# Kernel tuning notes

Measured on AMD Instinct MI355X. Metric: run time of the kernel, lower is better.

Reference implementation:

```python
import jax, jax.numpy as jnp
import numpy as np

B, S, D, H, FF = 4, 1024, 1024, 16, 4096
DH = D // H
EPS = 1e-5  # torch LayerNorm default


def _layernorm(x, g, b):
    m = jnp.mean(x, axis=-1, keepdims=True)
    v = jnp.mean((x - m) ** 2, axis=-1, keepdims=True)
    return (x - m) * jax.lax.rsqrt(v + EPS) * g + b


def setup_inputs() -> dict:
    key = jax.random.key(0)
    ks = jax.random.split(key, 8)
    init = lambda k, shape: jax.random.normal(k, shape, jnp.float32) * 0.02
    return {
        "x": jax.random.normal(ks[0], (B, S, D), jnp.float32),
        "Wq": init(ks[1], (D, D)), "bq": jnp.zeros((D,), jnp.float32),
        "Wk": init(ks[2], (D, D)), "bk": jnp.zeros((D,), jnp.float32),
        "Wv": init(ks[3], (D, D)), "bv": jnp.zeros((D,), jnp.float32),
        "Wo": init(ks[4], (D, D)), "bo": jnp.zeros((D,), jnp.float32),
        "ln1_g": jnp.ones((D,), jnp.float32), "ln1_b": jnp.zeros((D,), jnp.float32),
        "W1": init(ks[5], (D, FF)), "b1": jnp.zeros((FF,), jnp.float32),
        "W2": init(ks[6], (FF, D)), "b2": jnp.zeros((D,), jnp.float32),
        "ln2_g": jnp.ones((D,), jnp.float32), "ln2_b": jnp.zeros((D,), jnp.float32),
    }


def reference(x, Wq, bq, Wk, bk, Wv, bv, Wo, bo,
              ln1_g, ln1_b, W1, b1, W2, b2, ln2_g, ln2_b):
    Bx, Sx, _ = x.shape

    def heads(w, b):  # [B,S,D] -> [B,H,S,DH]
        return (x @ w + b).reshape(Bx, Sx, H, DH).transpose(0, 2, 1, 3)

    q, k, v = heads(Wq, bq), heads(Wk, bk), heads(Wv, bv)
    scores = jnp.einsum('bhqd,bhkd->bhqk', q, k) / jnp.sqrt(jnp.float32(DH))
    causal = jnp.tril(jnp.ones((Sx, Sx), bool))
    scores = jnp.where(causal[None, None], scores, jnp.float32(-1e9))
    attn = jax.nn.softmax(scores, axis=-1)           # [B,H,S,S]
    ctx = jnp.einsum('bhqk,bhkd->bqhd', attn, v).reshape(Bx, Sx, D)
    attn_out = ctx @ Wo + bo
    h = _layernorm(x + attn_out, ln1_g, ln1_b)
    ff = jax.nn.relu(h @ W1 + b1) @ W2 + b2
    y = _layernorm(h + ff, ln2_g, ln2_b)
    return (y, attn)
```

## Files before the change

### kernel.cpp

```cpp
#include <hip/hip_runtime.h>
#include <cstdint>


#define T_B 4
#define T_S 1024
#define T_D 1024
#define T_H 16
#define T_DH 64
#define T_FF 4096
#define T_TOK (T_B * T_S)

typedef __attribute__((ext_vector_type(8))) short bf16x8;
typedef __attribute__((ext_vector_type(4))) float f32x4;

__device__ __forceinline__ short f2bf(float f) {
  uint32_t u = __float_as_uint(f);
  u += 0x7FFFu + ((u >> 16) & 1u);
  return (short)(u >> 16);
}

__device__ __forceinline__ float bf2f(short s) {
  return __uint_as_float(((uint32_t)(unsigned short)s) << 16);
}

__device__ __forceinline__ void async_copy16(void* lds, const void* g) {
  __builtin_amdgcn_global_load_lds(
      (__attribute__((address_space(1))) uint32_t*)(uintptr_t)g,
      (__attribute__((address_space(3))) uint32_t*)(uint32_t)(uintptr_t)lds,
      16, 0, 0);
}

__device__ __forceinline__ void stage_ring(char* base, const char* gA0,
                                           const char* gA1, const char* gB0,
                                           const char* gB1, int koffB, int wid) {
  async_copy16(base + (wid << 10), gA0 + koffB);
  async_copy16(base + 4096 + (wid << 10), gA1 + koffB);
  async_copy16(base + 8192 + (wid << 10), gB0 + koffB);
  async_copy16(base + 12288 + (wid << 10), gB1 + koffB);
}

__device__ __forceinline__ void compute32(const short* As, const short* Bs,
                                          int wm, int wn, int quad, int r16,
                                          f32x4 acc[4][4]) {
  bf16x8 av[4], bv[4];
#pragma unroll
  for (int i = 0; i < 4; ++i) {
    av[i] = *(const bf16x8*)(As + ((wm + i * 16 + r16) << 5) + (quad << 3));
    bv[i] = *(const bf16x8*)(Bs + ((wn + i * 16 + r16) << 5) + (quad << 3));
  }
#pragma unroll
  for (int mi = 0; mi < 4; ++mi)
#pragma unroll
    for (int ni = 0; ni < 4; ++ni)
      acc[mi][ni] = __builtin_amdgcn_mfma_f32_16x16x32_bf16(av[mi], bv[ni],
                                                            acc[mi][ni], 0, 0, 0);
}

__device__ __forceinline__ void mfma_loop_ring(
    const short* __restrict__ A, int lda, const short* __restrict__ Bm, int ldb,
    int kLen, int m0, int n0, char* smem, f32x4 acc[4][4]) {
  const int t = threadIdx.x;
  const int lane = t & 63, wid = t >> 6;
  const int wm = (wid >> 1) << 6, wn = (wid & 1) << 6;
  const int quad = lane >> 4, r16 = lane & 15;
  const int row0 = t >> 2, cb0 = (t & 3) << 4;
  const char* gA0 = (const char*)A + (((size_t)(m0 + row0) * lda) << 1) + cb0;
  const char* gA1 = gA0 + ((size_t)lda << 7);
  const char* gB0 = (const char*)Bm + (((size_t)(n0 + row0) * ldb) << 1) + cb0;
  const char* gB1 = gB0 + ((size_t)ldb << 7);

  const f32x4 zf = {0.f, 0.f, 0.f, 0.f};
#pragma unroll
  for (int i = 0; i < 4; ++i)
#pragma unroll
    for (int j = 0; j < 4; ++j) acc[i][j] = zf;

  const int nIter = kLen >> 5;
  stage_ring(smem, gA0, gA1, gB0, gB1, 0, wid);
  stage_ring(smem + 16384, gA0, gA1, gB0, gB1, 64, wid);
  asm volatile("s_waitcnt vmcnt(4)" ::: "memory");
  __builtin_amdgcn_s_barrier();
  __builtin_amdgcn_sched_barrier(0);

  int cur = 0;
  for (int it = 0; it < nIter; ++it) {
    const int k2 = (it + 2) << 5;
    if (k2 < kLen) {
      int nb = cur + 2;
      if (nb >= 3) nb -= 3;
      stage_ring(smem + nb * 16384, gA0, gA1, gB0, gB1, k2 << 1, wid);
    }
    const short* As = (const short*)(smem + cur * 16384);
    const short* Bs = (const short*)(smem + cur * 16384 + 8192);
    compute32(As, Bs, wm, wn, quad, r16, acc);
    if (k2 < kLen)
      asm volatile("s_waitcnt vmcnt(4)" ::: "memory");
    else
      asm volatile("s_waitcnt vmcnt(0)" ::: "memory");
    __builtin_amdgcn_s_barrier();
    __builtin_amdgcn_sched_barrier(0);
    ++cur;
    if (cur >= 3) cur -= 3;
  }
}

template <int MODE>
__global__ __launch_bounds__(256) void gemm_dense(
    const short* __restrict__ A, const short* __restrict__ Bw, int K, int N,
    const float* __restrict__ bias0, const float* __restrict__ bias1,
    const float* __restrict__ bias2, short* __restrict__ outb0,
    short* __restrict__ outb1, short* __restrict__ outb2) {
  __shared__ __align__(16) char smem[49152];
  const int m0 = blockIdx.x << 7, n0 = blockIdx.y << 7;
  f32x4 acc[4][4];
  mfma_loop_ring(A, K, Bw, K, K, m0, n0, smem, acc);

  const int t = threadIdx.x;
  const int lane = t & 63, wid = t >> 6;
  const int wm = (wid >> 1) << 6, wn = (wid & 1) << 6;
  const int quad = lane >> 4, r16 = lane & 15;

  if constexpr (MODE == 0) {
    const int which = n0 >> 10;
    const float* bias = (which == 0) ? bias0 : (which == 1) ? bias1 : bias2;
    if (which < 2) {
      short* outp = (which == 0) ? outb0 : outb1;
#pragma unroll
      for (int mi = 0; mi < 4; ++mi) {
#pragma unroll
        for (int ni = 0; ni < 4; ++ni) {
          const int col = n0 + wn + ni * 16 + r16;
          const int c10 = col & 1023;
          const float bb = bias[c10];
          const int hh = c10 >> 6, dh = col & 63;
#pragma unroll
          for (int reg = 0; reg < 4; ++reg) {
            const int row = m0 + wm + mi * 16 + quad * 4 + reg;
            const int b = row >> 10, s = row & 1023;
            outp[((((size_t)b * T_H + hh) * T_S) + s) * T_DH + dh] =
                f2bf(acc[mi][ni][reg] + bb);
          }
        }
      }
    } else {
      __syncthreads();
      short* vtile = (short*)smem;
#pragma unroll
      for (int mi = 0; mi < 4; ++mi)
#pragma unroll
        for (int ni = 0; ni < 4; ++ni) {
          const int c = wn + ni * 16 + r16;
          const float bb = bias[(n0 + c) & 1023];
#pragma unroll
          for (int reg = 0; reg < 4; ++reg) {
            const int r = wm + mi * 16 + quad * 4 + reg;
            vtile[c * 136 + r] = f2bf(acc[mi][ni][reg] + bb);
          }
        }
      __syncthreads();
      const int b = m0 >> 10, s0 = m0 & 1023;
      const int c = t >> 1, half = t & 1;
      const int c10 = (n0 + c) & 1023;
      const int hh = c10 >> 6, dh = c10 & 63;
      short* dst = outb2 + (((size_t)b * T_H + hh) * T_DH + dh) * T_S + s0 + half * 64;
      const short* srcl = vtile + c * 136 + half * 64;
#pragma unroll
      for (int j = 0; j < 8; ++j)
        *(bf16x8*)(dst + j * 8) = *(const bf16x8*)(srcl + j * 8);
    }
  } else {
#pragma unroll
    for (int mi = 0; mi < 4; ++mi)
#pragma unroll
      for (int ni = 0; ni < 4; ++ni) {
        const int col = n0 + wn + ni * 16 + r16;
        const float bb = bias0[col];
#pragma unroll
        for (int reg = 0; reg < 4; ++reg) {
          const int row = m0 + wm + mi * 16 + quad * 4 + reg;
          outb0[(size_t)row * N + col] = f2bf(fmaxf(acc[mi][ni][reg] + bb, 0.f));
        }
      }
  }
}

__global__ __launch_bounds__(256) void gemm_splitk(
    const short* __restrict__ A, const short* __restrict__ Bw, int K, int N,
    int kc, float* __restrict__ outp) {
  __shared__ __align__(16) char smem[49152];
  const int m0 = blockIdx.x << 7, n0 = blockIdx.y << 7, z = blockIdx.z;
  f32x4 acc[4][4];
  mfma_loop_ring(A + (size_t)z * kc, K, Bw + (size_t)z * kc, K, kc, m0, n0,
                 smem, acc);
  float* o = outp + (size_t)z * T_TOK * N;
  const int t = threadIdx.x;
  const int lane = t & 63, wid = t >> 6;
  const int wm = (wid >> 1) << 6, wn = (wid & 1) << 6;
  const int quad = lane >> 4, r16 = lane & 15;
#pragma unroll
  for (int mi = 0; mi < 4; ++mi)
#pragma unroll
    for (int ni = 0; ni < 4; ++ni) {
      const int col = n0 + wn + ni * 16 + r16;
#pragma unroll
      for (int reg = 0; reg < 4; ++reg) {
        const int row = m0 + wm + mi * 16 + quad * 4 + reg;
        o[(size_t)row * N + col] = acc[mi][ni][reg];
      }
    }
}

__global__ __launch_bounds__(256) void attn_pass1(
    const short* __restrict__ qg, const short* __restrict__ kg,
    const short* __restrict__ vg, short* __restrict__ ctx,
    float* __restrict__ rsinv_g) {
  const int qb = blockIdx.x;
  const int bh = blockIdx.y;
  const int b = bh >> 4, h = bh & 15;
  const int m0 = qb << 7;
  __shared__ __align__(16) short Es[4 * 128 * 32];
  __shared__ float rsbuf[2][128];
  const int t = threadIdx.x;
  const int lane = t & 63, wid = t >> 6;
  const int quad = lane >> 4, r16 = lane & 15;
  const int wm = (wid >> 1) << 6, wn = (wid & 1) << 6;
  const int pvm = wid << 5;

  const short* Qbh = qg + (size_t)bh * T_S * T_DH;
  const short* Kbh = kg + (size_t)bh * T_S * T_DH;
  const short* Vbh = vg + (size_t)bh * T_DH * T_S;

  bf16x8 qf[4][2];
#pragma unroll
  for (int mi = 0; mi < 4; ++mi)
#pragma unroll
    for (int ksd = 0; ksd < 2; ++ksd)
      qf[mi][ksd] = *(const bf16x8*)(Qbh + (size_t)(m0 + wm + mi * 16 + r16) * T_DH +
                                     ksd * 32 + quad * 8);

  float rs[4][4];
#pragma unroll
  for (int i = 0; i < 4; ++i)
#pragma unroll
    for (int j = 0; j < 4; ++j) rs[i][j] = 0.f;
  const f32x4 zf = {0.f, 0.f, 0.f, 0.f};
  f32x4 accp[2][4];
#pragma unroll
  for (int i = 0; i < 2; ++i)
#pragma unroll
    for (int j = 0; j < 4; ++j) accp[i][j] = zf;

  for (int kt = 0; kt <= qb; ++kt) {
    f32x4 accs[4][4];
#pragma unroll
    for (int i = 0; i < 4; ++i)
#pragma unroll
      for (int j = 0; j < 4; ++j) accs[i][j] = zf;
#pragma unroll
    for (int ksd = 0; ksd < 2; ++ksd) {
      bf16x8 bv[4];
#pragma unroll
      for (int ni = 0; ni < 4; ++ni)
        bv[ni] = *(const bf16x8*)(Kbh + (size_t)(kt * 128 + wn + ni * 16 + r16) * T_DH +
                                  ksd * 32 + quad * 8);
#pragma unroll
      for (int mi = 0; mi < 4; ++mi)
#pragma unroll
        for (int ni = 0; ni < 4; ++ni)
          accs[mi][ni] = __builtin_amdgcn_mfma_f32_16x16x32_bf16(
              qf[mi][ksd], bv[ni], accs[mi][ni], 0, 0, 0);
    }
    __syncthreads();
    const bool diag = (kt == qb);
#pragma unroll
    for (int mi = 0; mi < 4; ++mi) {
#pragma unroll
      for (int ni = 0; ni < 4; ++ni) {
        const int cbase = wn + ni * 16;
        const int kse = cbase >> 5;
        const int sin = (cbase & 31) + r16;
        short* ep = Es + kse * 4096 + (wm + mi * 16 + quad * 4) * 32 + sin;
        const int colw = cbase + r16;
#pragma unroll
        for (int reg = 0; reg < 4; ++reg) {
          float e = __expf(accs[mi][ni][reg] * 0.125f);
          if (diag && colw > (wm + mi * 16 + quad * 4 + reg)) e = 0.f;
          ep[reg * 32] = f2bf(e);
          rs[mi][reg] += e;
        }
      }
    }
    __syncthreads();
#pragma unroll
    for (int ks = 0; ks < 4; ++ks) {
      bf16x8 av[2], bvv[4];
#pragma unroll
      for (int i = 0; i < 2; ++i)
        av[i] = *(const bf16x8*)(Es + ks * 4096 + (pvm + i * 16 + r16) * 32 + quad * 8);
#pragma unroll
      for (int ni = 0; ni < 4; ++ni)
        bvv[ni] = *(const bf16x8*)(Vbh + (size_t)(ni * 16 + r16) * T_S + kt * 128 +
                                   ks * 32 + quad * 8);
#pragma unroll
      for (int i = 0; i < 2; ++i)
#pragma unroll
        for (int ni = 0; ni < 4; ++ni)
          accp[i][ni] = __builtin_amdgcn_mfma_f32_16x16x32_bf16(av[i], bvv[ni],
                                                                accp[i][ni], 0, 0, 0);
    }
  }

#pragma unroll
  for (int mi = 0; mi < 4; ++mi)
#pragma unroll
    for (int reg = 0; reg < 4; ++reg) {
#pragma unroll
      for (int d = 1; d < 16; d <<= 1)
        rs[mi][reg] += __shfl_xor(rs[mi][reg], d, 64);
    }
  if (r16 == 0) {
#pragma unroll
    for (int mi = 0; mi < 4; ++mi)
#pragma unroll
      for (int reg = 0; reg < 4; ++reg)
        rsbuf[wid & 1][wm + mi * 16 + quad * 4 + reg] = rs[mi][reg];
  }
  __syncthreads();
  if (t < 128) {
    const float iv = 1.f / (rsbuf[0][t] + rsbuf[1][t]);
    rsbuf[0][t] = iv;
    rsinv_g[(size_t)bh * T_S + m0 + t] = iv;
  }
  __syncthreads();
#pragma unroll
  for (int i = 0; i < 2; ++i)
#pragma unroll
    for (int ni = 0; ni < 4; ++ni) {
#pragma unroll
      for (int reg = 0; reg < 4; ++reg) {
        const int row = pvm + i * 16 + quad * 4 + reg;
        const float iv = rsbuf[0][row];
        ctx[((size_t)b * T_S + m0 + row) * T_D + h * 64 + ni * 16 + r16] =
            f2bf(accp[i][ni][reg] * iv);
      }
    }
}

__global__ __launch_bounds__(256) void attn_pass2(
    const short* __restrict__ qg, const short* __restrict__ kg,
    const float* __restrict__ rsinv_g, float* __restrict__ attn) {
  const int qb = blockIdx.x, kt = blockIdx.y, bh = blockIdx.z;
  float* out = attn + ((size_t)bh * T_S + qb * 128) * T_S + kt * 128;
  const int t = threadIdx.x;
  if (kt > qb) {
    const float4 z4 = {0.f, 0.f, 0.f, 0.f};
#pragma unroll
    for (int j = 0; j < 16; ++j) {
      const int id = t + j * 256;
      ((float4*)(out + (size_t)(id >> 5) * T_S))[id & 31] = z4;
    }
    return;
  }
  const int lane = t & 63, wid = t >> 6;
  const int quad = lane >> 4, r16 = lane & 15;
  const int wm = (wid >> 1) << 6, wn = (wid & 1) << 6;
  const short* Qbh = qg + (size_t)bh * T_S * T_DH;
  const short* Kbh = kg + (size_t)bh * T_S * T_DH;
  const f32x4 zf = {0.f, 0.f, 0.f, 0.f};
  f32x4 accs[4][4];
#pragma unroll
  for (int i = 0; i < 4; ++i)
#pragma unroll
    for (int j = 0; j < 4; ++j) accs[i][j] = zf;
#pragma unroll
  for (int ksd = 0; ksd < 2; ++ksd) {
    bf16x8 aq[4], bv[4];
#pragma unroll
    for (int mi = 0; mi < 4; ++mi)
      aq[mi] = *(const bf16x8*)(Qbh + (size_t)(qb * 128 + wm + mi * 16 + r16) * T_DH +
                                ksd * 32 + quad * 8);
#pragma unroll
    for (int ni = 0; ni < 4; ++ni)
      bv[ni] = *(const bf16x8*)(Kbh + (size_t)(kt * 128 + wn + ni * 16 + r16) * T_DH +
                                ksd * 32 + quad * 8);
#pragma unroll
    for (int mi = 0; mi < 4; ++mi)
#pragma unroll
      for (int ni = 0; ni < 4; ++ni)
        accs[mi][ni] = __builtin_amdgcn_mfma_f32_16x16x32_bf16(aq[mi], bv[ni],
                                                               accs[mi][ni], 0, 0, 0);
  }
  const bool diag = (kt == qb);
#pragma unroll
  for (int mi = 0; mi < 4; ++mi)
#pragma unroll
    for (int ni = 0; ni < 4; ++ni) {
      const int col = wn + ni * 16 + r16;
#pragma unroll
      for (int reg = 0; reg < 4; ++reg) {
        const int rowt = wm + mi * 16 + quad * 4 + reg;
        const float iv = rsinv_g[(size_t)bh * T_S + qb * 128 + rowt];
        float e = __expf(accs[mi][ni][reg] * 0.125f) * iv;
        if (diag && col > rowt) e = 0.f;
        out[(size_t)rowt * T_S + col] = e;
      }
    }
}

__global__ __launch_bounds__(256) void ln_multi(
    const float* __restrict__ a32, const short* __restrict__ a16,
    const float* __restrict__ parts, int nparts, const float* __restrict__ bias,
    const float* __restrict__ g, const float* __restrict__ be,
    float* __restrict__ outf, short* __restrict__ outb) {
  const int row = blockIdx.x;
  const int t = threadIdx.x;
  float4 x;
  if (a32 != nullptr) {
    x = ((const float4*)(a32 + (size_t)row * T_D))[t];
  } else {
    const short4 s4 = ((const short4*)(a16 + (size_t)row * T_D))[t];
    x.x = bf2f(s4.x); x.y = bf2f(s4.y); x.z = bf2f(s4.z); x.w = bf2f(s4.w);
  }
  const float4 bv = ((const float4*)bias)[t];
  x.x += bv.x; x.y += bv.y; x.z += bv.z; x.w += bv.w;
  for (int p = 0; p < nparts; ++p) {
    const float4 v =
        ((const float4*)(parts + (size_t)p * T_TOK * T_D + (size_t)row * T_D))[t];
    x.x += v.x; x.y += v.y; x.z += v.z; x.w += v.w;
  }
  float sum = x.x + x.y + x.z + x.w;
  float sq = x.x * x.x + x.y * x.y + x.z * x.z + x.w * x.w;
  __shared__ float reds[4], redq[4];
  const int lane = t & 63, wid = t >> 6;
#pragma unroll
  for (int o = 32; o > 0; o >>= 1) {
    sum += __shfl_down(sum, o, 64);
    sq += __shfl_down(sq, o, 64);
  }
  if (lane == 0) { reds[wid] = sum; redq[wid] = sq; }
  __syncthreads();
  sum = reds[0] + reds[1] + reds[2] + reds[3];
  sq = redq[0] + redq[1] + redq[2] + redq[3];
  const float mean = sum * (1.f / T_D);
  const float var = sq * (1.f / T_D) - mean * mean;
  const float rstd = rsqrtf(var + 1e-5f);
  const float4 gg = ((const float4*)g)[t];
  const float4 bb = ((const float4*)be)[t];
  float4 y;
  y.x = (x.x - mean) * rstd * gg.x + bb.x;
  y.y = (x.y - mean) * rstd * gg.y + bb.y;
  y.z = (x.z - mean) * rstd * gg.z + bb.z;
  y.w = (x.w - mean) * rstd * gg.w + bb.w;
  if (outf != nullptr) ((float4*)(outf + (size_t)row * T_D))[t] = y;
  if (outb != nullptr) {
    short4 o4;
    o4.x = f2bf(y.x); o4.y = f2bf(y.y); o4.z = f2bf(y.z); o4.w = f2bf(y.w);
    ((short4*)(outb + (size_t)row * T_D))[t] = o4;
  }
}

__global__ __launch_bounds__(256) void prep_kernel(
    const float* __restrict__ x, short* __restrict__ xb,
    const float* __restrict__ Wq, const float* __restrict__ Wk,
    const float* __restrict__ Wv, const float* __restrict__ Wo,
    const float* __restrict__ W1, const float* __restrict__ W2,
    short* __restrict__ Wqkv_t, short* __restrict__ Wo_t,
    short* __restrict__ W1_t, short* __restrict__ W2_t) {
  int id = blockIdx.x;
  const int t = threadIdx.x;
  if (id < 4096) {
    const int i = id * 256 + t;
    const float4 v = ((const float4*)x)[i];
    short4 o;
    o.x = f2bf(v.x); o.y = f2bf(v.y); o.z = f2bf(v.z); o.w = f2bf(v.w);
    ((short4*)xb)[i] = o;
    return;
  }
  id -= 4096;
  const float* src;
  short* dst;
  int R, C;
  if (id < 1024) { src = Wq; dst = Wqkv_t; R = 1024; C = 1024; }
  else if (id < 2048) { id -= 1024; src = Wk; dst = Wqkv_t + 1024 * 1024; R = 1024; C = 1024; }
  else if (id < 3072) { id -= 2048; src = Wv; dst = Wqkv_t + 2 * 1024 * 1024; R = 1024; C = 1024; }
  else if (id < 4096) { id -= 3072; src = Wo; dst = Wo_t; R = 1024; C = 1024; }
  else if (id < 8192) { id -= 4096; src = W1; dst = W1_t; R = 1024; C = 4096; }
  else { id -= 8192; src = W2; dst = W2_t; R = 4096; C = 1024; }
  const int tilesC = C >> 5;
  const int r0 = (id / tilesC) << 5, c0 = (id % tilesC) << 5;
  __shared__ float tile[32][33];
  const int tx = t & 31, ty = t >> 5;
#pragma unroll
  for (int j = 0; j < 4; ++j)
    tile[ty + j * 8][tx] = src[(size_t)(r0 + ty + j * 8) * C + c0 + tx];
  __syncthreads();
#pragma unroll
  for (int j = 0; j < 4; ++j)
    dst[(size_t)(c0 + ty + j * 8) * R + r0 + tx] = f2bf(tile[tx][ty + j * 8]);
}

extern "C" void kernel_launch(void* const* d_in, const int* in_sizes, int n_in,
                              void* d_out, int out_size, void* d_ws,
                              size_t ws_size, hipStream_t stream) {
  const float* x = (const float*)d_in[0];
  const float* Wq = (const float*)d_in[1];
  const float* bq = (const float*)d_in[2];
  const float* Wk = (const float*)d_in[3];
  const float* bk = (const float*)d_in[4];
  const float* Wv = (const float*)d_in[5];
  const float* bv = (const float*)d_in[6];
  const float* Wo = (const float*)d_in[7];
  const float* bo = (const float*)d_in[8];
  const float* ln1g = (const float*)d_in[9];
  const float* ln1b = (const float*)d_in[10];
  const float* W1 = (const float*)d_in[11];
  const float* b1 = (const float*)d_in[12];
  const float* W2 = (const float*)d_in[13];
  const float* b2 = (const float*)d_in[14];
  const float* ln2g = (const float*)d_in[15];
  const float* ln2b = (const float*)d_in[16];
  (void)in_sizes; (void)n_in; (void)out_size; (void)ws_size;

  float* y_out = (float*)d_out;
  float* attn = (float*)d_out + (size_t)T_TOK * T_D;

  char* w = (char*)d_ws;
  size_t off = 0;
  auto alloc = [&](size_t bytes) -> void* {
    void* p = w + off;
    off += (bytes + 255) & ~(size_t)255;
    return p;
  };
  short* xb     = (short*)alloc((size_t)T_TOK * T_D * 2);
  short* Wqkv_t = (short*)alloc((size_t)3 * T_D * T_D * 2);
  short* Wo_t   = (short*)alloc((size_t)T_D * T_D * 2);
  short* W1_t   = (short*)alloc((size_t)T_FF * T_D * 2);
  short* W2_t   = (short*)alloc((size_t)T_D * T_FF * 2);
  short* qb_    = (short*)alloc((size_t)T_TOK * T_D * 2);
  short* kb_    = (short*)alloc((size_t)T_TOK * T_D * 2);
  short* vtb    = (short*)alloc((size_t)T_TOK * T_D * 2);
  short* ctx    = (short*)alloc((size_t)T_TOK * T_D * 2);
  short* hb     = (short*)alloc((size_t)T_TOK * T_D * 2);
  short* ff1    = (short*)alloc((size_t)T_TOK * T_FF * 2);
  float* rsinv  = (float*)alloc((size_t)T_H * T_B * T_S * 4);
  float* woP    = (float*)alloc((size_t)2 * T_TOK * T_D * 4);
  float* ffP    = (float*)alloc((size_t)2 * T_TOK * T_D * 4);

  prep_kernel<<<dim3(16384), dim3(256), 0, stream>>>(
      x, xb, Wq, Wk, Wv, Wo, W1, W2, Wqkv_t, Wo_t, W1_t, W2_t);

  gemm_dense<0><<<dim3(32, 24), dim3(256), 0, stream>>>(
      xb, Wqkv_t, T_D, 3072, bq, bk, bv, qb_, kb_, vtb);
  attn_pass1<<<dim3(8, 64), dim3(256), 0, stream>>>(qb_, kb_, vtb, ctx, rsinv);
  attn_pass2<<<dim3(8, 8, 64), dim3(256), 0, stream>>>(qb_, kb_, rsinv, attn);

  gemm_splitk<<<dim3(32, 8, 2), dim3(256), 0, stream>>>(ctx, Wo_t, T_D, T_D, 512, woP);
  ln_multi<<<dim3(4096), dim3(256), 0, stream>>>(x, nullptr, woP, 2, bo, ln1g,
                                                 ln1b, nullptr, hb);

  gemm_dense<2><<<dim3(32, 32), dim3(256), 0, stream>>>(
      hb, W1_t, T_D, T_FF, b1, nullptr, nullptr, ff1, nullptr, nullptr);
  gemm_splitk<<<dim3(32, 8, 2), dim3(256), 0, stream>>>(ff1, W2_t, T_FF, T_D, 2048, ffP);
  ln_multi<<<dim3(4096), dim3(256), 0, stream>>>(nullptr, hb, ffP, 2, b2, ln2g,
                                                 ln2b, y_out, nullptr);
}
```

Measured before the change: 623.1 us.

## Pre-pack weight tiles into MFMA fragment order for contiguous B loads

The weight-conversion kernel now writes each transposed bf16 weight as packed 128x32 tiles laid out in the exact per-lane MFMA fragment order. The GEMM B-stage then streams one contiguous 8 KB block per k-step, and each lane reads its fragments with a simple linear LDS offset. This is meant to replace strided row gathers with fully coalesced global loads, cut address arithmetic, and possibly reduce LDS bank conflicts on B reads. In exchange the packing is more complex and half the threads sit idle in the write-out, and every consumer of these weights must use the packed layout.

```diff
diff --git a/kernel.cpp b/kernel.cpp
--- a/kernel.cpp
+++ b/kernel.cpp
@@ -32,21 +32,22 @@
 
 __device__ __forceinline__ void stage_ring(char* base, const char* gA0,
                                            const char* gA1, const char* gB0,
-                                           const char* gB1, int koffB, int wid) {
-  async_copy16(base + (wid << 10), gA0 + koffB);
-  async_copy16(base + 4096 + (wid << 10), gA1 + koffB);
+                                           const char* gB1, int koffA, int koffB,
+                                           int wid) {
+  async_copy16(base + (wid << 10), gA0 + koffA);
+  async_copy16(base + 4096 + (wid << 10), gA1 + koffA);
   async_copy16(base + 8192 + (wid << 10), gB0 + koffB);
   async_copy16(base + 12288 + (wid << 10), gB1 + koffB);
 }
 
-__device__ __forceinline__ void compute32(const short* As, const short* Bs,
-                                          int wm, int wn, int quad, int r16,
-                                          f32x4 acc[4][4]) {
+__device__ __forceinline__ void compute32(const char* slot, int wm, int quad,
+                                          int r16, int boffB, f32x4 acc[4][4]) {
+  const short* As = (const short*)slot;
   bf16x8 av[4], bv[4];
 #pragma unroll
   for (int i = 0; i < 4; ++i) {
     av[i] = *(const bf16x8*)(As + ((wm + i * 16 + r16) << 5) + (quad << 3));
-    bv[i] = *(const bf16x8*)(Bs + ((wn + i * 16 + r16) << 5) + (quad << 3));
+    bv[i] = *(const bf16x8*)(slot + 8192 + boffB + (i << 10));
   }
 #pragma unroll
   for (int mi = 0; mi < 4; ++mi)
@@ -57,17 +58,20 @@
 }
 
 __device__ __forceinline__ void mfma_loop_ring(
-    const short* __restrict__ A, int lda, const short* __restrict__ Bm, int ldb,
-    int kLen, int m0, int n0, char* smem, f32x4 acc[4][4]) {
+    const short* __restrict__ A, int lda, const char* __restrict__ Bpack,
+    int ldbK, int kBase, int kLen, int m0, int n0, char* smem,
+    f32x4 acc[4][4]) {
   const int t = threadIdx.x;
   const int lane = t & 63, wid = t >> 6;
   const int wm = (wid >> 1) << 6, wn = (wid & 1) << 6;
   const int quad = lane >> 4, r16 = lane & 15;
+  const int boffB = ((wn >> 6) << 12) + (lane << 4);
   const int row0 = t >> 2, cb0 = (t & 3) << 4;
   const char* gA0 = (const char*)A + (((size_t)(m0 + row0) * lda) << 1) + cb0;
   const char* gA1 = gA0 + ((size_t)lda << 7);
-  const char* gB0 = (const char*)Bm + (((size_t)(n0 + row0) * ldb) << 1) + cb0;
-  const char* gB1 = gB0 + ((size_t)ldb << 7);
+  const char* gB0 = Bpack +
+      ((size_t)(n0 >> 7) * (ldbK >> 5) + (kBase >> 5)) * 8192 + (t << 4);
+  const char* gB1 = gB0 + 4096;
 
   const f32x4 zf = {0.f, 0.f, 0.f, 0.f};
 #pragma unroll
@@ -76,8 +80,8 @@
     for (int j = 0; j < 4; ++j) acc[i][j] = zf;
 
   const int nIter = kLen >> 5;
-  stage_ring(smem, gA0, gA1, gB0, gB1, 0, wid);
-  stage_ring(smem + 16384, gA0, gA1, gB0, gB1, 64, wid);
+  stage_ring(smem, gA0, gA1, gB0, gB1, 0, 0, wid);
+  stage_ring(smem + 16384, gA0, gA1, gB0, gB1, 64, 8192, wid);
   asm volatile("s_waitcnt vmcnt(4)" ::: "memory");
   __builtin_amdgcn_s_barrier();
   __builtin_amdgcn_sched_barrier(0);
@@ -88,11 +92,9 @@
     if (k2 < kLen) {
       int nb = cur + 2;
       if (nb >= 3) nb -= 3;
-      stage_ring(smem + nb * 16384, gA0, gA1, gB0, gB1, k2 << 1, wid);
-    }
-    const short* As = (const short*)(smem + cur * 16384);
-    const short* Bs = (const short*)(smem + cur * 16384 + 8192);
-    compute32(As, Bs, wm, wn, quad, r16, acc);
+      stage_ring(smem + nb * 16384, gA0, gA1, gB0, gB1, k2 << 1, k2 << 8, wid);
+    }
+    compute32(smem + cur * 16384, wm, quad, r16, boffB, acc);
     if (k2 < kLen)
       asm volatile("s_waitcnt vmcnt(4)" ::: "memory");
     else
@@ -113,7 +115,7 @@
   __shared__ __align__(16) char smem[49152];
   const int m0 = blockIdx.x << 7, n0 = blockIdx.y << 7;
   f32x4 acc[4][4];
-  mfma_loop_ring(A, K, Bw, K, K, m0, n0, smem, acc);
+  mfma_loop_ring(A, K, (const char*)Bw, K, 0, K, m0, n0, smem, acc);
 
   const int t = threadIdx.x;
   const int lane = t & 63, wid = t >> 6;
@@ -190,7 +192,7 @@
   __shared__ __align__(16) char smem[49152];
   const int m0 = blockIdx.x << 7, n0 = blockIdx.y << 7, z = blockIdx.z;
   f32x4 acc[4][4];
-  mfma_loop_ring(A + (size_t)z * kc, K, Bw + (size_t)z * kc, K, kc, m0, n0,
+  mfma_loop_ring(A + (size_t)z * kc, K, (const char*)Bw, K, z * kc, kc, m0, n0,
                  smem, acc);
   float* o = outp + (size_t)z * T_TOK * N;
   const int t = threadIdx.x;
@@ -494,9 +496,17 @@
   for (int j = 0; j < 4; ++j)
     tile[ty + j * 8][tx] = src[(size_t)(r0 + ty + j * 8) * C + c0 + tx];
   __syncthreads();
-#pragma unroll
-  for (int j = 0; j < 4; ++j)
-    dst[(size_t)(c0 + ty + j * 8) * R + r0 + tx] = f2bf(tile[tx][ty + j * 8]);
+  if (t < 128) {
+    const int b = t >> 2, c = t & 3;
+    bf16x8 v8;
+#pragma unroll
+    for (int j = 0; j < 8; ++j) v8[j] = f2bf(tile[c * 8 + j][b]);
+    const int p = c0 >> 7, h = (c0 >> 6) & 1;
+    const int g = ((c0 & 63) >> 4) + (b >> 4), r = b & 15;
+    char* dp = (char*)dst + ((size_t)p * (R >> 5) + (r0 >> 5)) * 8192 +
+               h * 4096 + g * 1024 + c * 256 + r * 16;
+    *(bf16x8*)dp = v8;
+  }
 }
 
 extern "C" void kernel_launch(void* const* d_in, const int* in_sizes, int n_in,
```

Result: no change. 616.8 us (-1.0%).
